# Kernel optimization log

Hardware: AMD Instinct MI355X
Metric: run time of the kernel (lower is better)

## Reference

```python
import jax, jax.numpy as jnp
import numpy as np

B, H, W, C = 32, 128, 128, 64
MX, MY = 32, 32  # modes_x, modes_y


def setup_inputs() -> dict:
    key = jax.random.key(0)
    k1, k2, k3, k4 = jax.random.split(key, 4)
    # glorot-ish scales for the spectral and conv weights
    wscale = (2.0 / (C + C)) ** 0.5
    return {
        "x": jax.random.normal(k1, (B, H, W, C), dtype=jnp.float32),
        "w_real": jax.random.normal(k2, (MX, MY, C, C), dtype=jnp.float32) * wscale,
        "w_imag": jax.random.normal(k3, (MX, MY, C, C), dtype=jnp.float32) * wscale,
        "conv_w": jax.random.normal(k4, (C, C), dtype=jnp.float32) * wscale,
        "conv_b": jnp.zeros((C,), dtype=jnp.float32),
    }


def reference(x, w_real, w_imag, conv_w, conv_b):
    # Complex spectral mixing weights [MX, MY, Cin, Cout]
    weights = jax.lax.complex(w_real, w_imag)
    # tf.signal.fft2d transforms the innermost TWO axes of [B,H,W,C],
    # i.e. axes (W, C); jnp.fft.fft2 default axes=(-2,-1) matches exactly.
    x_ft = jnp.fft.fft2(x.astype(jnp.complex64))           # [B,H,W,C] complex64
    # Mode truncation on axes (H, W), as in the original code.
    x_ft_trunc = x_ft[:, :MX, :MY, :]                      # [B,MX,MY,C]
    # Complex channel-mixing einsum over the low modes.
    x_ft_proc = jnp.einsum('bxyi,xyio->bxyo', x_ft_trunc, weights)  # [B,MX,MY,C]
    # Zero-pad back to the full grid on (H, W).
    x_ft_padded = jnp.pad(x_ft_proc,
                          ((0, 0), (0, H - MX), (0, W - MY), (0, 0)))
    # IFFT again over innermost two axes (W, C), take real part.
    x_spec = jnp.real(jnp.fft.ifft2(x_ft_padded))          # [B,H,W,C] float32
    # 1x1 conv (pointwise channel mix) + bias on the raw input.
    x_local = jnp.einsum('bhwi,io->bhwo', x, conv_w) + conv_b
    return jax.nn.relu(x_spec + x_local)
```

## Files before the change

kernel.cpp:

```cpp
#include <hip/hip_runtime.h>

typedef __attribute__((ext_vector_type(8))) short short8;
typedef __attribute__((ext_vector_type(4))) short bf16x4;
typedef __attribute__((ext_vector_type(4))) float f32x4;
typedef unsigned short ushort_t;

#define MFMA(a, b, c) __builtin_amdgcn_mfma_f32_16x16x32_bf16((a), (b), (c), 0, 0, 0)

constexpr int NB = 32, NHt = 128, NWd = 128, NC = 64, MX = 32;
constexpr float TWO_PI = 6.28318530717958647692f;

constexpr size_t TAB_T3 = 32768;
constexpr size_t TAB_T4 = 49152;
constexpr size_t XY_OFF = 65536;

__device__ inline ushort_t f2bf(float f) {
    union { float f; unsigned int u; } v; v.f = f;
    unsigned int r = v.u + 0x7FFFu + ((v.u >> 16) & 1u);
    return (ushort_t)(r >> 16);
}
__device__ inline int sxor(int row) { return ((row >> 3) & 3) << 4; }

__global__ __launch_bounds__(512) void k1_fwd(
    const float* __restrict__ x, char* __restrict__ tabs, ushort_t* __restrict__ XY)
{
    const int b = blockIdx.x, h = blockIdx.y;
    const int tid = threadIdx.x, lane = tid & 63, wv = tid >> 6;
    constexpr int SXT  = 0;
    constexpr int M1RE = 17408;
    constexpr int M1IM = 17408 + 4608;
    __shared__ __align__(16) char sm[26624];

    if (b == 0 && h == 0) {
        {
            int nt2 = tid >> 7, ks2 = (tid >> 6) & 1, l = tid & 63;
            int cc2 = (l & 15) + 16 * nt2, ob = (l >> 4) * 8 + 32 * ks2;
            short8 vre, vim;
            #pragma unroll
            for (int j = 0; j < 8; ++j) {
                float a = (float)(((ob + j) * cc2) & 63) * (TWO_PI / 64.f);
                float s, c; __sincosf(a, &s, &c);
                vre[j] = (short)f2bf(c); vim[j] = (short)f2bf(s);
            }
            *reinterpret_cast<short8*>(tabs + TAB_T3 + tid * 32)      = vre;
            *reinterpret_cast<short8*>(tabs + TAB_T3 + tid * 32 + 16) = vim;
        }
        {
            int mt2 = tid >> 6, l = tid & 63;
            int w = (l & 15) + 16 * mt2, ub = (l >> 4) * 8;
            short8 vre, vim;
            #pragma unroll
            for (int j = 0; j < 8; ++j) {
                float a = (float)((w * (ub + j)) & 127) * (TWO_PI / 128.f);
                float s, c; __sincosf(a, &s, &c);
                vre[j] = (short)f2bf(c * 0.0001220703125f);
                vim[j] = (short)f2bf(s * 0.0001220703125f);
            }
            *reinterpret_cast<short8*>(tabs + TAB_T4 + tid * 32)      = vre;
            *reinterpret_cast<short8*>(tabs + TAB_T4 + tid * 32 + 16) = vim;
        }
    }

    const float* xs = x + ((size_t)(b * NHt + h)) * (NWd * NC);
    #pragma unroll
    for (int i = 0; i < 4; ++i) {
        int idx = tid + 512 * i;
        int w = idx >> 4, c4 = (idx & 15) * 4;
        f32x4 v = *reinterpret_cast<const f32x4*>(xs + w * 64 + c4);
        #pragma unroll
        for (int j = 0; j < 4; ++j)
            *(ushort_t*)(sm + SXT + (c4 + j) * 272 + ((w * 2) ^ sxor(c4 + j))) = f2bf(v[j]);
    }
    __syncthreads();

    const int mt = wv >> 2, nt = wv & 3;
    f32x4 m1r = {0.f,0.f,0.f,0.f}, m1i = {0.f,0.f,0.f,0.f};
    const int cc = (lane & 15) + 16 * nt;
    const int uu = (lane & 15) + 16 * mt;
    #pragma unroll
    for (int ks = 0; ks < 4; ++ks) {
        short8 bfrag = *reinterpret_cast<const short8*>(
            sm + SXT + cc * 272 + (((lane >> 4) * 16 + 64 * ks) ^ sxor(cc)));
        int wb = (lane >> 4) * 8 + 32 * ks;
        short8 are, aim;
        #pragma unroll
        for (int j = 0; j < 8; ++j) {
            float a = (float)((uu * (wb + j)) & 127) * (TWO_PI / 128.f);
            float s, c; __sincosf(a, &s, &c);
            are[j] = (short)f2bf(c); aim[j] = (short)f2bf(-s);
        }
        m1r = MFMA(are, bfrag, m1r);
        m1i = MFMA(aim, bfrag, m1i);
    }
    #pragma unroll
    for (int r = 0; r < 4; ++r) {
        int u = (lane >> 4) * 4 + r + 16 * mt;
        int c = (lane & 15) + 16 * nt;
        *(ushort_t*)(sm + M1RE + u * 144 + c * 2) = f2bf(m1r[r]);
        *(ushort_t*)(sm + M1IM + u * 144 + c * 2) = f2bf(m1i[r]);
    }
    __syncthreads();

    f32x4 xP = {0.f,0.f,0.f,0.f}, xQ = {0.f,0.f,0.f,0.f}, xI = {0.f,0.f,0.f,0.f};
    const int kk = (lane & 15) + 16 * nt;
    #pragma unroll
    for (int ks = 0; ks < 2; ++ks) {
        short8 are = *reinterpret_cast<const short8*>(
            sm + M1RE + ((lane & 15) + 16 * mt) * 144 + (lane >> 4) * 16 + 64 * ks);
        short8 aim = *reinterpret_cast<const short8*>(
            sm + M1IM + ((lane & 15) + 16 * mt) * 144 + (lane >> 4) * 16 + 64 * ks);
        int cb2 = (lane >> 4) * 8 + 32 * ks;
        short8 bre, bim;
        #pragma unroll
        for (int j = 0; j < 8; ++j) {
            float a = (float)((kk * (cb2 + j)) & 63) * (TWO_PI / 64.f);
            float s, c; __sincosf(a, &s, &c);
            bre[j] = (short)f2bf(c); bim[j] = (short)f2bf(-s);
        }
        xP = MFMA(are, bre, xP);
        xQ = MFMA(aim, bim, xQ);
        xI = MFMA(are, bim, xI);
        xI = MFMA(aim, bre, xI);
    }
    #pragma unroll
    for (int r = 0; r < 4; ++r) {
        int u = (lane >> 4) * 4 + r + 16 * mt;
        int k = (lane & 15) + 16 * nt;
        *(ushort_t*)(sm + SXT + 0    + u * 128 + k * 2) = f2bf(xP[r] - xQ[r]);
        *(ushort_t*)(sm + SXT + 4096 + u * 128 + k * 2) = f2bf(xI[r]);
    }
    __syncthreads();

    {
        int u = tid >> 4, comp = (tid >> 3) & 1, k8 = (tid & 7) * 8;
        short8 v = *reinterpret_cast<const short8*>(sm + SXT + comp * 4096 + u * 128 + k8 * 2);
        size_t hu = (size_t)(h * 32 + u);
        *reinterpret_cast<short8*>(XY + ((hu * 2 + comp) * 32 + b) * 64 + k8) = v;
    }
}

__global__ __launch_bounds__(256) void k2_fused(
    const float* __restrict__ wre, const float* __restrict__ wim,
    ushort_t* __restrict__ XY,
    const float* __restrict__ x, const float* __restrict__ cw,
    const float* __restrict__ cb, float* __restrict__ out)
{
    const int bid = blockIdx.x;
    const int tid = threadIdx.x, lane = tid & 63, wv = tid >> 6;
    __shared__ __align__(16) char sm[36096];

    if (bid < 1024) {
        const int h = bid >> 5, u = bid & 31;
        constexpr int XRE = 0, XIM = 4608, WTR = 9216, WTI = 18432;
        const size_t hu = (size_t)(h * 32 + u);

        #pragma unroll
        for (int it = 0; it < 2; ++it) {
            int row = (tid >> 3) + 32 * it;
            int comp = row >> 5, bb = row & 31, k8 = (tid & 7) * 8;
            short8 v = *reinterpret_cast<const short8*>(XY + ((hu * 2 + comp) * 32 + bb) * 64 + k8);
            *reinterpret_cast<short8*>(sm + (comp ? XIM : XRE) + bb * 144 + k8 * 2) = v;
        }
        const float* wr = wre + hu * 4096;
        const float* wi = wim + hu * 4096;
        #pragma unroll
        for (int i = 0; i < 4; ++i) {
            int idx = tid + 256 * i;
            int k = idx >> 4, o4 = (idx & 15) * 4;
            f32x4 vr = __builtin_nontemporal_load(reinterpret_cast<const f32x4*>(wr + k * 64 + o4));
            f32x4 vi = __builtin_nontemporal_load(reinterpret_cast<const f32x4*>(wi + k * 64 + o4));
            #pragma unroll
            for (int j = 0; j < 4; ++j) {
                int o = o4 + j, koff = (k * 2) ^ sxor(o);
                *(ushort_t*)(sm + WTR + o * 144 + koff) = f2bf(vr[j]);
                *(ushort_t*)(sm + WTI + o * 144 + koff) = f2bf(vi[j]);
            }
        }
        __syncthreads();

        const int mt = wv >> 1;
        f32x4 yRe[2], yIm[2];
        #pragma unroll
        for (int half = 0; half < 2; ++half) {
            const int nt = (wv & 1) * 2 + half;
            const int oo = (lane & 15) + 16 * nt;
            f32x4 yP = {0.f,0.f,0.f,0.f}, yQ = {0.f,0.f,0.f,0.f}, yI = {0.f,0.f,0.f,0.f};
            #pragma unroll
            for (int ks = 0; ks < 2; ++ks) {
                int woff = ((lane >> 4) * 16 + 64 * ks) ^ sxor(oo);
                short8 are = *reinterpret_cast<const short8*>(
                    sm + XRE + ((lane & 15) + 16 * mt) * 144 + (lane >> 4) * 16 + 64 * ks);
                short8 aim = *reinterpret_cast<const short8*>(
                    sm + XIM + ((lane & 15) + 16 * mt) * 144 + (lane >> 4) * 16 + 64 * ks);
                short8 bre = *reinterpret_cast<const short8*>(sm + WTR + oo * 144 + woff);
                short8 bim = *reinterpret_cast<const short8*>(sm + WTI + oo * 144 + woff);
                yP = MFMA(are, bre, yP); yQ = MFMA(aim, bim, yQ);
                yI = MFMA(are, bim, yI); yI = MFMA(aim, bre, yI);
            }
            #pragma unroll
            for (int r = 0; r < 4; ++r) { yRe[half][r] = yP[r] - yQ[r]; yIm[half][r] = yI[r]; }
        }
        __syncthreads();

        #pragma unroll
        for (int half = 0; half < 2; ++half) {
            const int nt = (wv & 1) * 2 + half;
            #pragma unroll
            for (int r = 0; r < 4; ++r) {
                int bb = (lane >> 4) * 4 + r + 16 * mt;
                int o = (lane & 15) + 16 * nt;
                *(ushort_t*)(sm + 0    + bb * 128 + o * 2) = f2bf(yRe[half][r]);
                *(ushort_t*)(sm + 4096 + bb * 128 + o * 2) = f2bf(yIm[half][r]);
            }
        }
        __syncthreads();

        #pragma unroll
        for (int it = 0; it < 2; ++it) {
            int flat = tid + 256 * it;
            short8 v = *reinterpret_cast<const short8*>(sm + flat * 16);
            *reinterpret_cast<short8*>(XY + hu * 4096 + flat * 8) = v;
        }
    } else {
        const int cid = bid - 1024;
        const int b = cid / 192, rem = cid % 192;
        const int h = MX + (rem >> 1), w0 = (rem & 1) * 64;
        constexpr int XB   = 0;
        constexpr int CWT  = 9216;
        constexpr int SCB  = 18432;
        constexpr int OUTB = 18688;

        const float* xs = x + (((size_t)(b * NHt + h)) * NWd + w0) * NC;
        #pragma unroll
        for (int i = 0; i < 4; ++i) {
            int idx = tid + 256 * i;
            int w = idx >> 4, c4 = (idx & 15) * 4;
            f32x4 v = *reinterpret_cast<const f32x4*>(xs + w * 64 + c4);
            bf16x4 pk = { (short)f2bf(v[0]), (short)f2bf(v[1]),
                          (short)f2bf(v[2]), (short)f2bf(v[3]) };
            *reinterpret_cast<bf16x4*>(sm + XB + w * 144 + c4 * 2) = pk;
        }
        #pragma unroll
        for (int i = 0; i < 4; ++i) {
            int ii = (tid >> 4) + 16 * i;
            #pragma unroll
            for (int j = 0; j < 4; ++j) {
                int o = (tid & 15) + 16 * j;
                *(ushort_t*)(sm + CWT + o * 144 + ii * 2) = f2bf(cw[ii * 64 + o]);
            }
        }
        if (tid < 64) ((float*)(sm + SCB))[tid] = cb[tid];
        __syncthreads();

        #pragma unroll
        for (int nt = 0; nt < 4; ++nt) {
            f32x4 acc = {0.f,0.f,0.f,0.f};
            #pragma unroll
            for (int ks = 0; ks < 2; ++ks) {
                short8 ah = *reinterpret_cast<const short8*>(
                    sm + XB + ((lane & 15) + 16 * wv) * 144 + (lane >> 4) * 16 + 64 * ks);
                short8 bw = *reinterpret_cast<const short8*>(
                    sm + CWT + ((lane & 15) + 16 * nt) * 144 + (lane >> 4) * 16 + 64 * ks);
                acc = MFMA(ah, bw, acc);
            }
            #pragma unroll
            for (int r = 0; r < 4; ++r) {
                int w = (lane >> 4) * 4 + r + 16 * wv;
                int c = (lane & 15) + 16 * nt;
                float v = acc[r] + ((const float*)(sm + SCB))[c];
                *(float*)(sm + OUTB + w * 272 + c * 4) = fmaxf(v, 0.0f);
            }
        }
        __syncthreads();

        float* orow = out + (((size_t)(b * NHt + h)) * NWd + w0) * NC;
        #pragma unroll
        for (int i = 0; i < 4; ++i) {
            int flat = tid + 256 * i;
            int w = flat >> 4, c4 = (flat & 15) * 4;
            f32x4 v = *reinterpret_cast<const f32x4*>(sm + OUTB + w * 272 + c4 * 4);
            __builtin_nontemporal_store(v, reinterpret_cast<f32x4*>(orow + w * 64 + c4));
        }
    }
}

__global__ __launch_bounds__(512, 4) void k3_spec(
    const float* __restrict__ x, const float* __restrict__ cw, const float* __restrict__ cb,
    const char* __restrict__ tabs, const ushort_t* __restrict__ XY, float* __restrict__ out)
{
    const int b = blockIdx.x, h = blockIdx.y;
    const int tid = threadIdx.x, lane = tid & 63, wv = tid >> 6;
    constexpr int ST_RE = 0, ST_IM = 5120;
    constexpr int XB   = 10240;
    constexpr int CWT  = 28672;
    constexpr int SCB  = 37888;
    constexpr int OUTB = 38144;
    constexpr int YRE  = 38144;
    constexpr int YIM  = 38144 + 4608;
    __shared__ __align__(16) char sm[72960];

    const float* xs = x + ((size_t)(b * NHt + h)) * (NWd * NC);
    f32x4 xv[4];
    #pragma unroll
    for (int i = 0; i < 4; ++i) {
        int idx = tid + 512 * i;
        int w = idx >> 4, c4 = (idx & 15) * 4;
        xv[i] = __builtin_nontemporal_load(reinterpret_cast<const f32x4*>(xs + w * 64 + c4));
    }
    short8 yv, gre, gim;
    {
        int u = tid >> 4, comp = (tid >> 3) & 1, o8 = (tid & 7) * 8;
        size_t hu = (size_t)(h * 32 + u);
        yv = *reinterpret_cast<const short8*>(XY + ((hu * 2 + comp) * 32 + b) * 64 + o8);
        const char* t4 = tabs + TAB_T4 + ((wv * 64 + lane) * 32);
        gre = *reinterpret_cast<const short8*>(t4);
        gim = *reinterpret_cast<const short8*>(t4 + 16);
    }

    #pragma unroll
    for (int i = 0; i < 4; ++i) {
        int idx = tid + 512 * i;
        int w = idx >> 4, c4 = (idx & 15) * 4;
        bf16x4 pk = { (short)f2bf(xv[i][0]), (short)f2bf(xv[i][1]),
                      (short)f2bf(xv[i][2]), (short)f2bf(xv[i][3]) };
        *reinterpret_cast<bf16x4*>(sm + XB + w * 144 + c4 * 2) = pk;
    }
    #pragma unroll
    for (int i = 0; i < 2; ++i) {
        int ii = (tid >> 4) + 32 * i;
        #pragma unroll
        for (int j = 0; j < 4; ++j) {
            int o = (tid & 15) + 16 * j;
            *(ushort_t*)(sm + CWT + o * 144 + ii * 2) = f2bf(cw[ii * 64 + o]);
        }
    }
    if (tid < 64) ((float*)(sm + SCB))[tid] = cb[tid];
    {
        int u = tid >> 4, comp = (tid >> 3) & 1, o8 = (tid & 7) * 8;
        *reinterpret_cast<short8*>(sm + (comp ? YIM : YRE) + u * 144 + o8 * 2) = yv;
    }
    __syncthreads();

    {
        const int mt = wv >> 2, nt = wv & 3;
        f32x4 sP = {0.f,0.f,0.f,0.f}, sQ = {0.f,0.f,0.f,0.f}, sI = {0.f,0.f,0.f,0.f};
        #pragma unroll
        for (int ks = 0; ks < 2; ++ks) {
            short8 are = *reinterpret_cast<const short8*>(
                sm + YRE + ((lane & 15) + 16 * mt) * 144 + (lane >> 4) * 16 + 64 * ks);
            short8 aim = *reinterpret_cast<const short8*>(
                sm + YIM + ((lane & 15) + 16 * mt) * 144 + (lane >> 4) * 16 + 64 * ks);
            const char* t3 = tabs + TAB_T3 + (((nt * 2 + ks) * 64 + lane) * 32);
            short8 bre = *reinterpret_cast<const short8*>(t3);
            short8 bim = *reinterpret_cast<const short8*>(t3 + 16);
            sP = MFMA(are, bre, sP); sQ = MFMA(aim, bim, sQ);
            sI = MFMA(are, bim, sI); sI = MFMA(aim, bre, sI);
        }
        #pragma unroll
        for (int r = 0; r < 4; ++r) {
            int u = (lane >> 4) * 4 + r + 16 * mt;
            int c = (lane & 15) + 16 * nt;
            *(ushort_t*)(sm + ST_RE + c * 80 + u * 2) = f2bf(sP[r] - sQ[r]);
            *(ushort_t*)(sm + ST_IM + c * 80 + u * 2) = f2bf(sI[r]);
        }
    }
    __syncthreads();

    #pragma unroll
    for (int nt = 0; nt < 4; ++nt) {
        f32x4 acc = {0.f,0.f,0.f,0.f};
        #pragma unroll
        for (int ks = 0; ks < 2; ++ks) {
            short8 ah = *reinterpret_cast<const short8*>(
                sm + XB + ((lane & 15) + 16 * wv) * 144 + (lane >> 4) * 16 + 64 * ks);
            short8 bw = *reinterpret_cast<const short8*>(
                sm + CWT + ((lane & 15) + 16 * nt) * 144 + (lane >> 4) * 16 + 64 * ks);
            acc = MFMA(ah, bw, acc);
        }
        short8 bre = *reinterpret_cast<const short8*>(
            sm + ST_RE + ((lane & 15) + 16 * nt) * 80 + (lane >> 4) * 16);
        short8 bim = *reinterpret_cast<const short8*>(
            sm + ST_IM + ((lane & 15) + 16 * nt) * 80 + (lane >> 4) * 16);
        f32x4 sp = {0.f,0.f,0.f,0.f}, sq = {0.f,0.f,0.f,0.f};
        sp = MFMA(gre, bre, sp);
        sq = MFMA(gim, bim, sq);
        #pragma unroll
        for (int r = 0; r < 4; ++r) {
            int w = (lane >> 4) * 4 + r + 16 * wv;
            int c = (lane & 15) + 16 * nt;
            float v = acc[r] + ((const float*)(sm + SCB))[c] + sp[r] - sq[r];
            *(float*)(sm + OUTB + w * 272 + c * 4) = fmaxf(v, 0.0f);
        }
    }
    __syncthreads();

    float* orow = out + ((size_t)(b * NHt + h)) * (NWd * NC);
    #pragma unroll
    for (int i = 0; i < 4; ++i) {
        int flat = tid + 512 * i;
        int w = flat >> 4, c4 = (flat & 15) * 4;
        f32x4 v = *reinterpret_cast<const f32x4*>(sm + OUTB + w * 272 + c4 * 4);
        __builtin_nontemporal_store(v, reinterpret_cast<f32x4*>(orow + w * 64 + c4));
    }
}

extern "C" void kernel_launch(void* const* d_in, const int* in_sizes, int n_in,
                              void* d_out, int out_size, void* d_ws, size_t ws_size,
                              hipStream_t stream) {
    const float* x      = (const float*)d_in[0];
    const float* w_real = (const float*)d_in[1];
    const float* w_imag = (const float*)d_in[2];
    const float* conv_w = (const float*)d_in[3];
    const float* conv_b = (const float*)d_in[4];
    float* out = (float*)d_out;

    char* tabs   = (char*)d_ws;
    ushort_t* XY = (ushort_t*)((char*)d_ws + XY_OFF);

    k1_fwd<<<dim3(NB, MX), 512, 0, stream>>>(x, tabs, XY);
    k2_fused<<<1024 + NB * (NHt - MX) * 2, 256, 0, stream>>>(
        w_real, w_imag, XY, x, conv_w, conv_b, out);
    k3_spec<<<dim3(NB, MX), 512, 0, stream>>>(x, conv_w, conv_b,
                                              (const char*)tabs, XY, out);
}
```

Baseline: 76.76 us.

## Spread local-conv rows across all three kernels to balance load

The pointwise conv+ReLU work for the non-spectral rows (h >= 32) was previously done entirely in k2. It is now split across the three launches: k1 handles 512 rows in quarter-row blocks, k2 handles 1536 rows in half-row blocks, and k3 handles the last 1024 rows as full-row blocks alongside the spectral blocks. The aim is to fill idle compute units in k1 and k3, which previously launched only 1024 blocks each. The cost is more blocks per launch, and the small quarter-row blocks in k1 each reload and convert the conv weights.

Result: faster. 73.29 us (-4.5%).

```diff
diff --git a/kernel.cpp b/kernel.cpp
--- a/kernel.cpp
+++ b/kernel.cpp
@@ -13,6 +13,7 @@
 constexpr size_t TAB_T3 = 32768;
 constexpr size_t TAB_T4 = 49152;
 constexpr size_t XY_OFF = 65536;
+
 
 __device__ inline ushort_t f2bf(float f) {
     union { float f; unsigned int u; } v; v.f = f;
@@ -21,121 +22,180 @@
 }
 __device__ inline int sxor(int row) { return ((row >> 3) & 3) << 4; }
 
-__global__ __launch_bounds__(512) void k1_fwd(
-    const float* __restrict__ x, char* __restrict__ tabs, ushort_t* __restrict__ XY)
+__global__ __launch_bounds__(512) void k1_fused(
+    const float* __restrict__ x, char* __restrict__ tabs, ushort_t* __restrict__ XY,
+    const float* __restrict__ cw, const float* __restrict__ cb, float* __restrict__ out)
 {
-    const int b = blockIdx.x, h = blockIdx.y;
+    const int bid = blockIdx.x;
     const int tid = threadIdx.x, lane = tid & 63, wv = tid >> 6;
-    constexpr int SXT  = 0;
-    constexpr int M1RE = 17408;
-    constexpr int M1IM = 17408 + 4608;
     __shared__ __align__(16) char sm[26624];
 
-    if (b == 0 && h == 0) {
+    if (bid < 1024) {
+        const int b = bid & 31, h = bid >> 5;
+        constexpr int SXT  = 0;
+        constexpr int M1RE = 17408;
+        constexpr int M1IM = 17408 + 4608;
+
+        if (bid == 0) {
+            {
+                int nt2 = tid >> 7, ks2 = (tid >> 6) & 1, l = tid & 63;
+                int cc2 = (l & 15) + 16 * nt2, ob = (l >> 4) * 8 + 32 * ks2;
+                short8 vre, vim;
+                #pragma unroll
+                for (int j = 0; j < 8; ++j) {
+                    float a = (float)(((ob + j) * cc2) & 63) * (TWO_PI / 64.f);
+                    float s, c; __sincosf(a, &s, &c);
+                    vre[j] = (short)f2bf(c); vim[j] = (short)f2bf(s);
+                }
+                *reinterpret_cast<short8*>(tabs + TAB_T3 + tid * 32)      = vre;
+                *reinterpret_cast<short8*>(tabs + TAB_T3 + tid * 32 + 16) = vim;
+            }
+            {
+                int mt2 = tid >> 6, l = tid & 63;
+                int w = (l & 15) + 16 * mt2, ub = (l >> 4) * 8;
+                short8 vre, vim;
+                #pragma unroll
+                for (int j = 0; j < 8; ++j) {
+                    float a = (float)((w * (ub + j)) & 127) * (TWO_PI / 128.f);
+                    float s, c; __sincosf(a, &s, &c);
+                    vre[j] = (short)f2bf(c * 0.0001220703125f);
+                    vim[j] = (short)f2bf(s * 0.0001220703125f);
+                }
+                *reinterpret_cast<short8*>(tabs + TAB_T4 + tid * 32)      = vre;
+                *reinterpret_cast<short8*>(tabs + TAB_T4 + tid * 32 + 16) = vim;
+            }
+        }
+
+        const float* xs = x + ((size_t)(b * NHt + h)) * (NWd * NC);
+        #pragma unroll
+        for (int i = 0; i < 4; ++i) {
+            int idx = tid + 512 * i;
+            int w = idx >> 4, c4 = (idx & 15) * 4;
+            f32x4 v = *reinterpret_cast<const f32x4*>(xs + w * 64 + c4);
+            #pragma unroll
+            for (int j = 0; j < 4; ++j)
+                *(ushort_t*)(sm + SXT + (c4 + j) * 272 + ((w * 2) ^ sxor(c4 + j))) = f2bf(v[j]);
+        }
+        __syncthreads();
+
+        const int mt = wv >> 2, nt = wv & 3;
+        f32x4 m1r = {0.f,0.f,0.f,0.f}, m1i = {0.f,0.f,0.f,0.f};
+        const int cc = (lane & 15) + 16 * nt;
+        const int uu = (lane & 15) + 16 * mt;
+        #pragma unroll
+        for (int ks = 0; ks < 4; ++ks) {
+            short8 bfrag = *reinterpret_cast<const short8*>(
+                sm + SXT + cc * 272 + (((lane >> 4) * 16 + 64 * ks) ^ sxor(cc)));
+            int wb = (lane >> 4) * 8 + 32 * ks;
+            short8 are, aim;
+            #pragma unroll
+            for (int j = 0; j < 8; ++j) {
+                float a = (float)((uu * (wb + j)) & 127) * (TWO_PI / 128.f);
+                float s, c; __sincosf(a, &s, &c);
+                are[j] = (short)f2bf(c); aim[j] = (short)f2bf(-s);
+            }
+            m1r = MFMA(are, bfrag, m1r);
+            m1i = MFMA(aim, bfrag, m1i);
+        }
+        #pragma unroll
+        for (int r = 0; r < 4; ++r) {
+            int u = (lane >> 4) * 4 + r + 16 * mt;
+            int c = (lane & 15) + 16 * nt;
+            *(ushort_t*)(sm + M1RE + u * 144 + c * 2) = f2bf(m1r[r]);
+            *(ushort_t*)(sm + M1IM + u * 144 + c * 2) = f2bf(m1i[r]);
+        }
+        __syncthreads();
+
+        f32x4 xP = {0.f,0.f,0.f,0.f}, xQ = {0.f,0.f,0.f,0.f}, xI = {0.f,0.f,0.f,0.f};
+        const int kk = (lane & 15) + 16 * nt;
+        #pragma unroll
+        for (int ks = 0; ks < 2; ++ks) {
+            short8 are = *reinterpret_cast<const short8*>(
+                sm + M1RE + ((lane & 15) + 16 * mt) * 144 + (lane >> 4) * 16 + 64 * ks);
+            short8 aim = *reinterpret_cast<const short8*>(
+                sm + M1IM + ((lane & 15) + 16 * mt) * 144 + (lane >> 4) * 16 + 64 * ks);
+            int cb2 = (lane >> 4) * 8 + 32 * ks;
+            short8 bre, bim;
+            #pragma unroll
+            for (int j = 0; j < 8; ++j) {
+                float a = (float)((kk * (cb2 + j)) & 63) * (TWO_PI / 64.f);
+                float s, c; __sincosf(a, &s, &c);
+                bre[j] = (short)f2bf(c); bim[j] = (short)f2bf(-s);
+            }
+            xP = MFMA(are, bre, xP);
+            xQ = MFMA(aim, bim, xQ);
+            xI = MFMA(are, bim, xI);
+            xI = MFMA(aim, bre, xI);
+        }
+        #pragma unroll
+        for (int r = 0; r < 4; ++r) {
+            int u = (lane >> 4) * 4 + r + 16 * mt;
+            int k = (lane & 15) + 16 * nt;
+            *(ushort_t*)(sm + SXT + 0    + u * 128 + k * 2) = f2bf(xP[r] - xQ[r]);
+            *(ushort_t*)(sm + SXT + 4096 + u * 128 + k * 2) = f2bf(xI[r]);
+        }
+        __syncthreads();
+
         {
-            int nt2 = tid >> 7, ks2 = (tid >> 6) & 1, l = tid & 63;
-            int cc2 = (l & 15) + 16 * nt2, ob = (l >> 4) * 8 + 32 * ks2;
-            short8 vre, vim;
-            #pragma unroll
-            for (int j = 0; j < 8; ++j) {
-                float a = (float)(((ob + j) * cc2) & 63) * (TWO_PI / 64.f);
-                float s, c; __sincosf(a, &s, &c);
-                vre[j] = (short)f2bf(c); vim[j] = (short)f2bf(s);
-            }
-            *reinterpret_cast<short8*>(tabs + TAB_T3 + tid * 32)      = vre;
-            *reinterpret_cast<short8*>(tabs + TAB_T3 + tid * 32 + 16) = vim;
-        }
+            int u = tid >> 4, comp = (tid >> 3) & 1, k8 = (tid & 7) * 8;
+            short8 v = *reinterpret_cast<const short8*>(sm + SXT + comp * 4096 + u * 128 + k8 * 2);
+            size_t hu = (size_t)(h * 32 + u);
+            *reinterpret_cast<short8*>(XY + ((hu * 2 + comp) * 32 + b) * 64 + k8) = v;
+        }
+    } else {
+        const int qid = bid - 1024;
+        const int r = qid >> 2;
+        const int b = r / 96, h = MX + r % 96, w0 = (qid & 3) * 32;
+        constexpr int XB   = 0;
+        constexpr int CWT  = 4608;
+        constexpr int SCB  = 13824;
+        constexpr int OUTB = 14080;
+
+        const float* xs = x + (((size_t)(b * NHt + h)) * NWd + w0) * NC;
         {
-            int mt2 = tid >> 6, l = tid & 63;
-            int w = (l & 15) + 16 * mt2, ub = (l >> 4) * 8;
-            short8 vre, vim;
-            #pragma unroll
-            for (int j = 0; j < 8; ++j) {
-                float a = (float)((w * (ub + j)) & 127) * (TWO_PI / 128.f);
-                float s, c; __sincosf(a, &s, &c);
-                vre[j] = (short)f2bf(c * 0.0001220703125f);
-                vim[j] = (short)f2bf(s * 0.0001220703125f);
-            }
-            *reinterpret_cast<short8*>(tabs + TAB_T4 + tid * 32)      = vre;
-            *reinterpret_cast<short8*>(tabs + TAB_T4 + tid * 32 + 16) = vim;
-        }
-    }
-
-    const float* xs = x + ((size_t)(b * NHt + h)) * (NWd * NC);
-    #pragma unroll
-    for (int i = 0; i < 4; ++i) {
-        int idx = tid + 512 * i;
-        int w = idx >> 4, c4 = (idx & 15) * 4;
-        f32x4 v = *reinterpret_cast<const f32x4*>(xs + w * 64 + c4);
-        #pragma unroll
-        for (int j = 0; j < 4; ++j)
-            *(ushort_t*)(sm + SXT + (c4 + j) * 272 + ((w * 2) ^ sxor(c4 + j))) = f2bf(v[j]);
-    }
-    __syncthreads();
-
-    const int mt = wv >> 2, nt = wv & 3;
-    f32x4 m1r = {0.f,0.f,0.f,0.f}, m1i = {0.f,0.f,0.f,0.f};
-    const int cc = (lane & 15) + 16 * nt;
-    const int uu = (lane & 15) + 16 * mt;
-    #pragma unroll
-    for (int ks = 0; ks < 4; ++ks) {
-        short8 bfrag = *reinterpret_cast<const short8*>(
-            sm + SXT + cc * 272 + (((lane >> 4) * 16 + 64 * ks) ^ sxor(cc)));
-        int wb = (lane >> 4) * 8 + 32 * ks;
-        short8 are, aim;
-        #pragma unroll
-        for (int j = 0; j < 8; ++j) {
-            float a = (float)((uu * (wb + j)) & 127) * (TWO_PI / 128.f);
-            float s, c; __sincosf(a, &s, &c);
-            are[j] = (short)f2bf(c); aim[j] = (short)f2bf(-s);
-        }
-        m1r = MFMA(are, bfrag, m1r);
-        m1i = MFMA(aim, bfrag, m1i);
-    }
-    #pragma unroll
-    for (int r = 0; r < 4; ++r) {
-        int u = (lane >> 4) * 4 + r + 16 * mt;
-        int c = (lane & 15) + 16 * nt;
-        *(ushort_t*)(sm + M1RE + u * 144 + c * 2) = f2bf(m1r[r]);
-        *(ushort_t*)(sm + M1IM + u * 144 + c * 2) = f2bf(m1i[r]);
-    }
-    __syncthreads();
-
-    f32x4 xP = {0.f,0.f,0.f,0.f}, xQ = {0.f,0.f,0.f,0.f}, xI = {0.f,0.f,0.f,0.f};
-    const int kk = (lane & 15) + 16 * nt;
-    #pragma unroll
-    for (int ks = 0; ks < 2; ++ks) {
-        short8 are = *reinterpret_cast<const short8*>(
-            sm + M1RE + ((lane & 15) + 16 * mt) * 144 + (lane >> 4) * 16 + 64 * ks);
-        short8 aim = *reinterpret_cast<const short8*>(
-            sm + M1IM + ((lane & 15) + 16 * mt) * 144 + (lane >> 4) * 16 + 64 * ks);
-        int cb2 = (lane >> 4) * 8 + 32 * ks;
-        short8 bre, bim;
-        #pragma unroll
-        for (int j = 0; j < 8; ++j) {
-            float a = (float)((kk * (cb2 + j)) & 63) * (TWO_PI / 64.f);
-            float s, c; __sincosf(a, &s, &c);
-            bre[j] = (short)f2bf(c); bim[j] = (short)f2bf(-s);
-        }
-        xP = MFMA(are, bre, xP);
-        xQ = MFMA(aim, bim, xQ);
-        xI = MFMA(are, bim, xI);
-        xI = MFMA(aim, bre, xI);
-    }
-    #pragma unroll
-    for (int r = 0; r < 4; ++r) {
-        int u = (lane >> 4) * 4 + r + 16 * mt;
-        int k = (lane & 15) + 16 * nt;
-        *(ushort_t*)(sm + SXT + 0    + u * 128 + k * 2) = f2bf(xP[r] - xQ[r]);
-        *(ushort_t*)(sm + SXT + 4096 + u * 128 + k * 2) = f2bf(xI[r]);
-    }
-    __syncthreads();
-
-    {
-        int u = tid >> 4, comp = (tid >> 3) & 1, k8 = (tid & 7) * 8;
-        short8 v = *reinterpret_cast<const short8*>(sm + SXT + comp * 4096 + u * 128 + k8 * 2);
-        size_t hu = (size_t)(h * 32 + u);
-        *reinterpret_cast<short8*>(XY + ((hu * 2 + comp) * 32 + b) * 64 + k8) = v;
+            int w = tid >> 4, c4 = (tid & 15) * 4;
+            f32x4 v = *reinterpret_cast<const f32x4*>(xs + w * 64 + c4);
+            bf16x4 pk = { (short)f2bf(v[0]), (short)f2bf(v[1]),
+                          (short)f2bf(v[2]), (short)f2bf(v[3]) };
+            *reinterpret_cast<bf16x4*>(sm + XB + w * 144 + c4 * 2) = pk;
+        }
+        #pragma unroll
+        for (int i = 0; i < 2; ++i) {
+            int ii = (tid >> 4) + 32 * i;
+            #pragma unroll
+            for (int j = 0; j < 4; ++j) {
+                int o = (tid & 15) + 16 * j;
+                *(ushort_t*)(sm + CWT + o * 144 + ii * 2) = f2bf(cw[ii * 64 + o]);
+            }
+        }
+        if (tid < 64) ((float*)(sm + SCB))[tid] = cb[tid];
+        __syncthreads();
+
+        const int mt = wv >> 2, nt = wv & 3;
+        f32x4 acc = {0.f,0.f,0.f,0.f};
+        #pragma unroll
+        for (int ks = 0; ks < 2; ++ks) {
+            short8 ah = *reinterpret_cast<const short8*>(
+                sm + XB + ((lane & 15) + 16 * mt) * 144 + (lane >> 4) * 16 + 64 * ks);
+            short8 bw = *reinterpret_cast<const short8*>(
+                sm + CWT + ((lane & 15) + 16 * nt) * 144 + (lane >> 4) * 16 + 64 * ks);
+            acc = MFMA(ah, bw, acc);
+        }
+        #pragma unroll
+        for (int r4 = 0; r4 < 4; ++r4) {
+            int w = (lane >> 4) * 4 + r4 + 16 * mt;
+            int c = (lane & 15) + 16 * nt;
+            float v = acc[r4] + ((const float*)(sm + SCB))[c];
+            *(float*)(sm + OUTB + w * 272 + c * 4) = fmaxf(v, 0.0f);
+        }
+        __syncthreads();
+
+        float* orow = out + (((size_t)(b * NHt + h)) * NWd + w0) * NC;
+        {
+            int w = tid >> 4, c4 = (tid & 15) * 4;
+            f32x4 v = *reinterpret_cast<const f32x4*>(sm + OUTB + w * 272 + c4 * 4);
+            __builtin_nontemporal_store(v, reinterpret_cast<f32x4*>(orow + w * 64 + c4));
+        }
     }
 }
 
@@ -222,9 +282,9 @@
             *reinterpret_cast<short8*>(XY + hu * 4096 + flat * 8) = v;
         }
     } else {
-        const int cid = bid - 1024;
-        const int b = cid / 192, rem = cid % 192;
-        const int h = MX + (rem >> 1), w0 = (rem & 1) * 64;
+        const int hid = bid - 1024;
+        const int r = 512 + (hid >> 1);
+        const int b = r / 96, h = MX + r % 96, w0 = (hid & 1) * 64;
         constexpr int XB   = 0;
         constexpr int CWT  = 9216;
         constexpr int SCB  = 18432;
@@ -264,10 +324,10 @@
                 acc = MFMA(ah, bw, acc);
             }
             #pragma unroll
-            for (int r = 0; r < 4; ++r) {
-                int w = (lane >> 4) * 4 + r + 16 * wv;
+            for (int r4 = 0; r4 < 4; ++r4) {
+                int w = (lane >> 4) * 4 + r4 + 16 * wv;
                 int c = (lane & 15) + 16 * nt;
-                float v = acc[r] + ((const float*)(sm + SCB))[c];
+                float v = acc[r4] + ((const float*)(sm + SCB))[c];
                 *(float*)(sm + OUTB + w * 272 + c * 4) = fmaxf(v, 0.0f);
             }
         }
@@ -284,123 +344,187 @@
     }
 }
 
-__global__ __launch_bounds__(512, 4) void k3_spec(
+__global__ __launch_bounds__(512, 4) void k3_fused(
     const float* __restrict__ x, const float* __restrict__ cw, const float* __restrict__ cb,
     const char* __restrict__ tabs, const ushort_t* __restrict__ XY, float* __restrict__ out)
 {
-    const int b = blockIdx.x, h = blockIdx.y;
+    const int bid = blockIdx.x;
     const int tid = threadIdx.x, lane = tid & 63, wv = tid >> 6;
-    constexpr int ST_RE = 0, ST_IM = 5120;
-    constexpr int XB   = 10240;
-    constexpr int CWT  = 28672;
-    constexpr int SCB  = 37888;
-    constexpr int OUTB = 38144;
-    constexpr int YRE  = 38144;
-    constexpr int YIM  = 38144 + 4608;
     __shared__ __align__(16) char sm[72960];
 
-    const float* xs = x + ((size_t)(b * NHt + h)) * (NWd * NC);
-    f32x4 xv[4];
-    #pragma unroll
-    for (int i = 0; i < 4; ++i) {
-        int idx = tid + 512 * i;
-        int w = idx >> 4, c4 = (idx & 15) * 4;
-        xv[i] = __builtin_nontemporal_load(reinterpret_cast<const f32x4*>(xs + w * 64 + c4));
-    }
-    short8 yv, gre, gim;
-    {
-        int u = tid >> 4, comp = (tid >> 3) & 1, o8 = (tid & 7) * 8;
-        size_t hu = (size_t)(h * 32 + u);
-        yv = *reinterpret_cast<const short8*>(XY + ((hu * 2 + comp) * 32 + b) * 64 + o8);
-        const char* t4 = tabs + TAB_T4 + ((wv * 64 + lane) * 32);
-        gre = *reinterpret_cast<const short8*>(t4);
-        gim = *reinterpret_cast<const short8*>(t4 + 16);
-    }
-
-    #pragma unroll
-    for (int i = 0; i < 4; ++i) {
-        int idx = tid + 512 * i;
-        int w = idx >> 4, c4 = (idx & 15) * 4;
-        bf16x4 pk = { (short)f2bf(xv[i][0]), (short)f2bf(xv[i][1]),
-                      (short)f2bf(xv[i][2]), (short)f2bf(xv[i][3]) };
-        *reinterpret_cast<bf16x4*>(sm + XB + w * 144 + c4 * 2) = pk;
-    }
-    #pragma unroll
-    for (int i = 0; i < 2; ++i) {
-        int ii = (tid >> 4) + 32 * i;
-        #pragma unroll
-        for (int j = 0; j < 4; ++j) {
-            int o = (tid & 15) + 16 * j;
-            *(ushort_t*)(sm + CWT + o * 144 + ii * 2) = f2bf(cw[ii * 64 + o]);
-        }
-    }
-    if (tid < 64) ((float*)(sm + SCB))[tid] = cb[tid];
-    {
-        int u = tid >> 4, comp = (tid >> 3) & 1, o8 = (tid & 7) * 8;
-        *reinterpret_cast<short8*>(sm + (comp ? YIM : YRE) + u * 144 + o8 * 2) = yv;
-    }
-    __syncthreads();
-
-    {
-        const int mt = wv >> 2, nt = wv & 3;
-        f32x4 sP = {0.f,0.f,0.f,0.f}, sQ = {0.f,0.f,0.f,0.f}, sI = {0.f,0.f,0.f,0.f};
-        #pragma unroll
-        for (int ks = 0; ks < 2; ++ks) {
-            short8 are = *reinterpret_cast<const short8*>(
-                sm + YRE + ((lane & 15) + 16 * mt) * 144 + (lane >> 4) * 16 + 64 * ks);
-            short8 aim = *reinterpret_cast<const short8*>(
-                sm + YIM + ((lane & 15) + 16 * mt) * 144 + (lane >> 4) * 16 + 64 * ks);
-            const char* t3 = tabs + TAB_T3 + (((nt * 2 + ks) * 64 + lane) * 32);
-            short8 bre = *reinterpret_cast<const short8*>(t3);
-            short8 bim = *reinterpret_cast<const short8*>(t3 + 16);
-            sP = MFMA(are, bre, sP); sQ = MFMA(aim, bim, sQ);
-            sI = MFMA(are, bim, sI); sI = MFMA(aim, bre, sI);
-        }
-        #pragma unroll
-        for (int r = 0; r < 4; ++r) {
-            int u = (lane >> 4) * 4 + r + 16 * mt;
-            int c = (lane & 15) + 16 * nt;
-            *(ushort_t*)(sm + ST_RE + c * 80 + u * 2) = f2bf(sP[r] - sQ[r]);
-            *(ushort_t*)(sm + ST_IM + c * 80 + u * 2) = f2bf(sI[r]);
-        }
-    }
-    __syncthreads();
-
-    #pragma unroll
-    for (int nt = 0; nt < 4; ++nt) {
-        f32x4 acc = {0.f,0.f,0.f,0.f};
-        #pragma unroll
-        for (int ks = 0; ks < 2; ++ks) {
-            short8 ah = *reinterpret_cast<const short8*>(
-                sm + XB + ((lane & 15) + 16 * wv) * 144 + (lane >> 4) * 16 + 64 * ks);
-            short8 bw = *reinterpret_cast<const short8*>(
-                sm + CWT + ((lane & 15) + 16 * nt) * 144 + (lane >> 4) * 16 + 64 * ks);
-            acc = MFMA(ah, bw, acc);
-        }
-        short8 bre = *reinterpret_cast<const short8*>(
-            sm + ST_RE + ((lane & 15) + 16 * nt) * 80 + (lane >> 4) * 16);
-        short8 bim = *reinterpret_cast<const short8*>(
-            sm + ST_IM + ((lane & 15) + 16 * nt) * 80 + (lane >> 4) * 16);
-        f32x4 sp = {0.f,0.f,0.f,0.f}, sq = {0.f,0.f,0.f,0.f};
-        sp = MFMA(gre, bre, sp);
-        sq = MFMA(gim, bim, sq);
-        #pragma unroll
-        for (int r = 0; r < 4; ++r) {
-            int w = (lane >> 4) * 4 + r + 16 * wv;
-            int c = (lane & 15) + 16 * nt;
-            float v = acc[r] + ((const float*)(sm + SCB))[c] + sp[r] - sq[r];
-            *(float*)(sm + OUTB + w * 272 + c * 4) = fmaxf(v, 0.0f);
-        }
-    }
-    __syncthreads();
-
-    float* orow = out + ((size_t)(b * NHt + h)) * (NWd * NC);
-    #pragma unroll
-    for (int i = 0; i < 4; ++i) {
-        int flat = tid + 512 * i;
-        int w = flat >> 4, c4 = (flat & 15) * 4;
-        f32x4 v = *reinterpret_cast<const f32x4*>(sm + OUTB + w * 272 + c4 * 4);
-        __builtin_nontemporal_store(v, reinterpret_cast<f32x4*>(orow + w * 64 + c4));
+    if (bid < 1024) {
+        const int b = bid & 31, h = bid >> 5;
+        constexpr int ST_RE = 0, ST_IM = 5120;
+        constexpr int XB   = 10240;
+        constexpr int CWT  = 28672;
+        constexpr int SCB  = 37888;
+        constexpr int OUTB = 38144;
+        constexpr int YRE  = 38144;
+        constexpr int YIM  = 38144 + 4608;
+
+        const float* xs = x + ((size_t)(b * NHt + h)) * (NWd * NC);
+        f32x4 xv[4];
+        #pragma unroll
+        for (int i = 0; i < 4; ++i) {
+            int idx = tid + 512 * i;
+            int w = idx >> 4, c4 = (idx & 15) * 4;
+            xv[i] = __builtin_nontemporal_load(reinterpret_cast<const f32x4*>(xs + w * 64 + c4));
+        }
+        short8 yv, gre, gim;
+        {
+            int u = tid >> 4, comp = (tid >> 3) & 1, o8 = (tid & 7) * 8;
+            size_t hu = (size_t)(h * 32 + u);
+            yv = *reinterpret_cast<const short8*>(XY + ((hu * 2 + comp) * 32 + b) * 64 + o8);
+            const char* t4 = tabs + TAB_T4 + ((wv * 64 + lane) * 32);
+            gre = *reinterpret_cast<const short8*>(t4);
+            gim = *reinterpret_cast<const short8*>(t4 + 16);
+        }
+
+        #pragma unroll
+        for (int i = 0; i < 4; ++i) {
+            int idx = tid + 512 * i;
+            int w = idx >> 4, c4 = (idx & 15) * 4;
+            bf16x4 pk = { (short)f2bf(xv[i][0]), (short)f2bf(xv[i][1]),
+                          (short)f2bf(xv[i][2]), (short)f2bf(xv[i][3]) };
+            *reinterpret_cast<bf16x4*>(sm + XB + w * 144 + c4 * 2) = pk;
+        }
+        #pragma unroll
+        for (int i = 0; i < 2; ++i) {
+            int ii = (tid >> 4) + 32 * i;
+            #pragma unroll
+            for (int j = 0; j < 4; ++j) {
+                int o = (tid & 15) + 16 * j;
+                *(ushort_t*)(sm + CWT + o * 144 + ii * 2) = f2bf(cw[ii * 64 + o]);
+            }
+        }
+        if (tid < 64) ((float*)(sm + SCB))[tid] = cb[tid];
+        {
+            int u = tid >> 4, comp = (tid >> 3) & 1, o8 = (tid & 7) * 8;
+            *reinterpret_cast<short8*>(sm + (comp ? YIM : YRE) + u * 144 + o8 * 2) = yv;
+        }
+        __syncthreads();
+
+        {
+            const int mt = wv >> 2, nt = wv & 3;
+            f32x4 sP = {0.f,0.f,0.f,0.f}, sQ = {0.f,0.f,0.f,0.f}, sI = {0.f,0.f,0.f,0.f};
+            #pragma unroll
+            for (int ks = 0; ks < 2; ++ks) {
+                short8 are = *reinterpret_cast<const short8*>(
+                    sm + YRE + ((lane & 15) + 16 * mt) * 144 + (lane >> 4) * 16 + 64 * ks);
+                short8 aim = *reinterpret_cast<const short8*>(
+                    sm + YIM + ((lane & 15) + 16 * mt) * 144 + (lane >> 4) * 16 + 64 * ks);
+                const char* t3 = tabs + TAB_T3 + (((nt * 2 + ks) * 64 + lane) * 32);
+                short8 bre = *reinterpret_cast<const short8*>(t3);
+                short8 bim = *reinterpret_cast<const short8*>(t3 + 16);
+                sP = MFMA(are, bre, sP); sQ = MFMA(aim, bim, sQ);
+                sI = MFMA(are, bim, sI); sI = MFMA(aim, bre, sI);
+            }
+            #pragma unroll
+            for (int r = 0; r < 4; ++r) {
+                int u = (lane >> 4) * 4 + r + 16 * mt;
+                int c = (lane & 15) + 16 * nt;
+                *(ushort_t*)(sm + ST_RE + c * 80 + u * 2) = f2bf(sP[r] - sQ[r]);
+                *(ushort_t*)(sm + ST_IM + c * 80 + u * 2) = f2bf(sI[r]);
+            }
+        }
+        __syncthreads();
+
+        #pragma unroll
+        for (int nt = 0; nt < 4; ++nt) {
+            f32x4 acc = {0.f,0.f,0.f,0.f};
+            #pragma unroll
+            for (int ks = 0; ks < 2; ++ks) {
+                short8 ah = *reinterpret_cast<const short8*>(
+                    sm + XB + ((lane & 15) + 16 * wv) * 144 + (lane >> 4) * 16 + 64 * ks);
+                short8 bw = *reinterpret_cast<const short8*>(
+                    sm + CWT + ((lane & 15) + 16 * nt) * 144 + (lane >> 4) * 16 + 64 * ks);
+                acc = MFMA(ah, bw, acc);
+            }
+            short8 bre = *reinterpret_cast<const short8*>(
+                sm + ST_RE + ((lane & 15) + 16 * nt) * 80 + (lane >> 4) * 16);
+            short8 bim = *reinterpret_cast<const short8*>(
+                sm + ST_IM + ((lane & 15) + 16 * nt) * 80 + (lane >> 4) * 16);
+            f32x4 sp = {0.f,0.f,0.f,0.f}, sq = {0.f,0.f,0.f,0.f};
+            sp = MFMA(gre, bre, sp);
+            sq = MFMA(gim, bim, sq);
+            #pragma unroll
+            for (int r = 0; r < 4; ++r) {
+                int w = (lane >> 4) * 4 + r + 16 * wv;
+                int c = (lane & 15) + 16 * nt;
+                float v = acc[r] + ((const float*)(sm + SCB))[c] + sp[r] - sq[r];
+                *(float*)(sm + OUTB + w * 272 + c * 4) = fmaxf(v, 0.0f);
+            }
+        }
+        __syncthreads();
+
+        float* orow = out + ((size_t)(b * NHt + h)) * (NWd * NC);
+        #pragma unroll
+        for (int i = 0; i < 4; ++i) {
+            int flat = tid + 512 * i;
+            int w = flat >> 4, c4 = (flat & 15) * 4;
+            f32x4 v = *reinterpret_cast<const f32x4*>(sm + OUTB + w * 272 + c4 * 4);
+            __builtin_nontemporal_store(v, reinterpret_cast<f32x4*>(orow + w * 64 + c4));
+        }
+    } else {
+        const int fid = bid - 1024;
+        const int r = 2048 + fid;
+        const int b = r / 96, h = MX + r % 96;
+        constexpr int XB   = 0;
+        constexpr int CWT  = 18432;
+        constexpr int SCB  = 27648;
+        constexpr int OUTB = 27904;
+
+        const float* xs = x + ((size_t)(b * NHt + h)) * (NWd * NC);
+        #pragma unroll
+        for (int i = 0; i < 4; ++i) {
+            int idx = tid + 512 * i;
+            int w = idx >> 4, c4 = (idx & 15) * 4;
+            f32x4 v = *reinterpret_cast<const f32x4*>(xs + w * 64 + c4);
+            bf16x4 pk = { (short)f2bf(v[0]), (short)f2bf(v[1]),
+                          (short)f2bf(v[2]), (short)f2bf(v[3]) };
+            *reinterpret_cast<bf16x4*>(sm + XB + w * 144 + c4 * 2) = pk;
+        }
+        #pragma unroll
+        for (int i = 0; i < 2; ++i) {
+            int ii = (tid >> 4) + 32 * i;
+            #pragma unroll
+            for (int j = 0; j < 4; ++j) {
+                int o = (tid & 15) + 16 * j;
+                *(ushort_t*)(sm + CWT + o * 144 + ii * 2) = f2bf(cw[ii * 64 + o]);
+            }
+        }
+        if (tid < 64) ((float*)(sm + SCB))[tid] = cb[tid];
+        __syncthreads();
+
+        #pragma unroll
+        for (int nt = 0; nt < 4; ++nt) {
+            f32x4 acc = {0.f,0.f,0.f,0.f};
+            #pragma unroll
+            for (int ks = 0; ks < 2; ++ks) {
+                short8 ah = *reinterpret_cast<const short8*>(
+                    sm + XB + ((lane & 15) + 16 * wv) * 144 + (lane >> 4) * 16 + 64 * ks);
+                short8 bw = *reinterpret_cast<const short8*>(
+                    sm + CWT + ((lane & 15) + 16 * nt) * 144 + (lane >> 4) * 16 + 64 * ks);
+                acc = MFMA(ah, bw, acc);
+            }
+            #pragma unroll
+            for (int r4 = 0; r4 < 4; ++r4) {
+                int w = (lane >> 4) * 4 + r4 + 16 * wv;
+                int c = (lane & 15) + 16 * nt;
+                float v = acc[r4] + ((const float*)(sm + SCB))[c];
+                *(float*)(sm + OUTB + w * 272 + c * 4) = fmaxf(v, 0.0f);
+            }
+        }
+        __syncthreads();
+
+        float* orow = out + ((size_t)(b * NHt + h)) * (NWd * NC);
+        #pragma unroll
+        for (int i = 0; i < 4; ++i) {
+            int flat = tid + 512 * i;
+            int w = flat >> 4, c4 = (flat & 15) * 4;
+            f32x4 v = *reinterpret_cast<const f32x4*>(sm + OUTB + w * 272 + c4 * 4);
+            __builtin_nontemporal_store(v, reinterpret_cast<f32x4*>(orow + w * 64 + c4));
+        }
     }
 }
 
@@ -417,9 +541,8 @@
     char* tabs   = (char*)d_ws;
     ushort_t* XY = (ushort_t*)((char*)d_ws + XY_OFF);
 
-    k1_fwd<<<dim3(NB, MX), 512, 0, stream>>>(x, tabs, XY);
-    k2_fused<<<1024 + NB * (NHt - MX) * 2, 256, 0, stream>>>(
-        w_real, w_imag, XY, x, conv_w, conv_b, out);
-    k3_spec<<<dim3(NB, MX), 512, 0, stream>>>(x, conv_w, conv_b,
+    k1_fused<<<1024 + 2048, 512, 0, stream>>>(x, tabs, XY, conv_w, conv_b, out);
+    k2_fused<<<1024 + 3072, 256, 0, stream>>>(w_real, w_imag, XY, x, conv_w, conv_b, out);
+    k3_fused<<<1024 + 1024, 512, 0, stream>>>(x, conv_w, conv_b,
                                               (const char*)tabs, XY, out);
 }
```
